# Kernel tuning notes

Hardware: AMD Instinct MI355X
Metric: run time of the kernel (lower is better)

Reference implementation:

```python
import jax, jax.numpy as jnp
import numpy as np

T = 1_000_000          # number of t_eval points (~1 year at 30 s)
N_ROOMS = 10
N = 12                 # 2 latent wall nodes + n_rooms
DT = 30.0              # seconds between t_eval points
LOAD_SCALE = 50.0      # physical_cooling_scaling: W/m^2 scale for sigmoid(loads)


def setup_inputs() -> dict:
    key = jax.random.key(0)
    k1, k2, k3, k4, k5 = jax.random.split(key, 5)
    t_eval = jnp.arange(T, dtype=jnp.float32) * DT
    x0 = 26.0 * jnp.ones((N,), jnp.float32)  # reset_iv: 26 C at every node
    # Stable slow RC dynamics: negative-definite-ish A with small coupling
    A = (-1e-5 * jnp.eye(N, dtype=jnp.float32)
         + 1e-6 * jax.random.normal(k1, (N, N), jnp.float32))
    B = 1e-6 * jax.random.normal(k2, (N, 1 + N_ROOMS), jnp.float32)
    Tout_data = 10.0 + 20.0 * jax.random.uniform(k3, (T,), jnp.float32)  # outdoor temp samples on t_eval grid
    loads_raw = jax.random.normal(k4, (2, N_ROOMS), jnp.float32)         # pre-sigmoid [cool; gain] loads
    room_areas = 10.0 + 40.0 * jax.random.uniform(k5, (N_ROOMS,), jnp.float32)
    return {"t_eval": t_eval, "x0": x0, "A": A, "B": B,
            "Tout_data": Tout_data, "loads_raw": loads_raw, "room_areas": room_areas}


def reference(t_eval, x0, A, B, Tout_data, loads_raw, room_areas):
    # transform + physical scaling of loads (self.transform = sigmoid)
    loads = jax.nn.sigmoid(loads_raw) * LOAD_SCALE
    cool_load, gain_load = loads[0], loads[1]
    action = 0.0  # no cooling policy -> self.action stays 0
    Q_area = -cool_load * action + gain_load            # [n_rooms]
    Q_watts = Q_area * room_areas                        # proportional_heating
    # u = [Tout; Q_watts] so B@u = B[:,0]*Tout + B[:,1:]@Q_watts (Q constant over t)
    b0 = B[:, 0]                                         # [N]
    Bq = B[:, 1:] @ Q_watts                              # [N], constant forcing
    h = t_eval[1] - t_eval[0]                            # uniform step
    # Linear interp of Tout: value at t_i, midpoint t_i+h/2, and t_{i+1}
    To_t = Tout_data[:-1]
    To_n = Tout_data[1:]
    To_m = 0.5 * (To_t + To_n)

    def f(x, To):  # dy/dt = A x + B u
        return A @ x + b0 * To + Bq

    def step(x, tou):
        to_t, to_m, to_n = tou
        k1 = f(x, to_t)
        k2 = f(x + 0.5 * h * k1, to_m)
        k3 = f(x + 0.5 * h * k2, to_m)
        k4 = f(x + h * k3, to_n)
        xn = x + (h / 6.0) * (k1 + 2.0 * k2 + 2.0 * k3 + k4)
        return xn, xn

    _, xs = jax.lax.scan(step, x0, (To_t, To_m, To_n))
    return jnp.concatenate([x0[None, :], xs], axis=0)  # [T, N]
```

## Files before the change

### kernel.cpp

```cpp
#include <hip/hip_runtime.h>
#include <math.h>


#define S_STEPS 999999
#define CH      8
#define BLK     512
#define NB      256
#define NLVL    9
#define NLOOK   16
#define NCHUNK  125000
#define LASTFULL 124998

#define OFF_MX  0
#define OFF_K   192
#define OFF_P2  312
#define OFF_PD  1608
#define OFF_AGG 3912
#define OFF_S   6984

__device__ inline void mm12(double* C, const double* A_, const double* B_, int t) {
  if (t < 144) {
    int i = t / 12, j = t % 12;
    double s = 0.0;
#pragma unroll
    for (int k = 0; k < 12; ++k) s += A_[i*12+k] * B_[k*12+j];
    C[t] = s;
  }
  __syncthreads();
}

__device__ inline void matvec12_s(const float* __restrict__ P,
                                  const float* in, float* out) {
#pragma unroll
  for (int i = 0; i < 12; ++i) {
    float acc = out[i];
#pragma unroll
    for (int j = 0; j < 12; ++j) acc = fmaf(P[i*12+j], in[j], acc);
    out[i] = acc;
  }
}

__global__ void setup_kernel(const float* __restrict__ t_eval,
                             const float* __restrict__ A,
                             const float* __restrict__ Bm,
                             const float* __restrict__ loads_raw,
                             const float* __restrict__ areas,
                             float* __restrict__ ws) {
  __shared__ double Md[144], T2[144], CUR[144], R4[144];
  __shared__ double H1[144], H2[144], H3[144], H4[144];
  __shared__ double cd[12], ald[12], bed[12], bqd[12], b0d[12];
  __shared__ double Kd[120];
  int t = threadIdx.x;
  double h = (double)t_eval[1] - (double)t_eval[0];
  if (t < 144) H1[t] = h * (double)A[t];
  if (t < 12) {
    b0d[t] = (double)Bm[t*11];
    double s = 0.0;
    for (int r = 0; r < 10; ++r) {
      double g = 50.0 / (1.0 + exp(-(double)loads_raw[10 + r]));
      s += (double)Bm[t*11 + 1 + r] * (g * (double)areas[r]);
    }
    bqd[t] = s;
  }
  if (t < 120) Kd[t] = 0.0;
  __syncthreads();
  mm12(H2, H1, H1, t);
  mm12(H3, H2, H1, t);
  mm12(H4, H2, H2, t);
  if (t < 12) {
    double hb=0,h2b=0,h3b=0,hb0=0,h2b0=0,h3b0=0;
    for (int k = 0; k < 12; ++k) {
      hb  += H1[t*12+k]*bqd[k]; h2b  += H2[t*12+k]*bqd[k]; h3b  += H3[t*12+k]*bqd[k];
      hb0 += H1[t*12+k]*b0d[k]; h2b0 += H2[t*12+k]*b0d[k]; h3b0 += H3[t*12+k]*b0d[k];
    }
    double h6 = h / 6.0;
    cd[t]  = h6*(6.0*bqd[t] + 3.0*hb + h2b + 0.25*h3b);
    ald[t] = h6*(3.0*b0d[t] + 2.0*hb0 + 0.75*h2b0 + 0.25*h3b0);
    bed[t] = h6*(3.0*b0d[t] + hb0 + 0.25*h2b0);
  }
  if (t < 144) {
    int i = t/12, j = t%12;
    Md[t] = (i==j ? 1.0 : 0.0) + H1[t] + 0.5*H2[t] + H3[t]/6.0 + H4[t]/24.0;
  }
  if (t < 144) CUR[t] = (t % 13 == 0) ? 1.0 : 0.0;
  __syncthreads();
  if (t < 192) {
    int i = t/16, j = t%16;
    float val = (j < 12) ? (float)Md[i*12+j]
              : (j == 12) ? (float)cd[i]
              : (j == 13) ? (float)ald[i]
              : (j == 14) ? (float)bed[i] : 0.f;
    ws[OFF_MX + t] = val;
  }
  for (int k = 0; k <= 8; ++k) {
    if (k > 0) {
      mm12(T2, CUR, Md, t);
      if (t < 144) CUR[t] = T2[t];
      __syncthreads();
    }
    if (t < 12 && k <= 7) {
      double sa=0, sb=0, sc=0;
      for (int j = 0; j < 12; ++j) {
        double m = CUR[t*12+j];
        sa += m*ald[j]; sb += m*bed[j]; sc += m*cd[j];
      }
      Kd[(8-k)*12 + t] += sa;
      Kd[(9-k)*12 + t] += sb;
      Kd[t]            += sc;
    }
    __syncthreads();
  }
  if (t < 120) ws[OFF_K + t] = (float)Kd[t];
  if (t < 144) ws[OFF_P2 + t] = (float)CUR[t];
  for (int l = 1; l <= 8; ++l) {
    mm12(T2, CUR, CUR, t);
    if (t < 144) CUR[t] = T2[t];
    __syncthreads();
    if (t < 144) ws[OFF_P2 + l*144 + t] = (float)CUR[t];
  }
  mm12(R4, CUR, CUR, t);
  if (t < 144) {
    ws[OFF_PD + t] = (t % 13 == 0) ? 1.f : 0.f;
    ws[OFF_PD + 144 + t] = (float)R4[t];
    CUR[t] = R4[t];
  }
  __syncthreads();
  for (int j = 2; j < NLOOK; ++j) {
    mm12(T2, CUR, R4, t);
    if (t < 144) CUR[t] = T2[t];
    __syncthreads();
    if (t < 144) ws[OFF_PD + j*144 + t] = (float)CUR[t];
  }
}

__global__ void __launch_bounds__(BLK) fold_scan(
    const float* __restrict__ cons, const float* __restrict__ To,
    const float* __restrict__ x0, float* __restrict__ sout,
    float* __restrict__ agg) {
  __shared__ float lw[BLK*13];
  int k = threadIdx.x, b = blockIdx.x;
  int g = b*BLK + k;
  int base = g*CH;
  bool fullc = (g <= LASTFULL);
  float to[9];
  if (fullc) {
    const float4* tp = reinterpret_cast<const float4*>(To + base);
    float4 a = tp[0], c = tp[1];
    to[0]=a.x; to[1]=a.y; to[2]=a.z; to[3]=a.w;
    to[4]=c.x; to[5]=c.y; to[6]=c.z; to[7]=c.w;
    to[8]=To[base+8];
  }
  float v[12];
  if (fullc) {
#pragma unroll
    for (int i = 0; i < 12; ++i) v[i] = cons[OFF_K + i];
#pragma unroll
    for (int s = 0; s < 9; ++s) {
      float ts = to[s];
#pragma unroll
      for (int i = 0; i < 12; ++i)
        v[i] = fmaf(cons[OFF_K + (s+1)*12 + i], ts, v[i]);
    }
  } else {
#pragma unroll
    for (int i = 0; i < 12; ++i) v[i] = 0.f;
  }
  if (g == 0) {
    float xi[12];
#pragma unroll
    for (int i = 0; i < 12; ++i) xi[i] = x0[i];
    matvec12_s(cons + OFF_P2, xi, v);
  }
#pragma unroll
  for (int i = 0; i < 12; ++i) lw[k*13+i] = v[i];
  __syncthreads();
#pragma unroll
  for (int l = 0; l < NLVL; ++l) {
    int off = 1 << l;
    float nb[12];
    bool act = (k >= off);
    if (act) {
#pragma unroll
      for (int i = 0; i < 12; ++i) nb[i] = lw[(k-off)*13 + i];
    }
    __syncthreads();
    if (act) {
      matvec12_s(cons + OFF_P2 + l*144, nb, v);
#pragma unroll
      for (int i = 0; i < 12; ++i) lw[k*13+i] = v[i];
    }
    __syncthreads();
  }
  float4* Sp = reinterpret_cast<float4*>(sout + (size_t)g*12);
  Sp[0] = make_float4(v[0],v[1],v[2],v[3]);
  Sp[1] = make_float4(v[4],v[5],v[6],v[7]);
  Sp[2] = make_float4(v[8],v[9],v[10],v[11]);
  if (k == BLK-1) {
#pragma unroll
    for (int i = 0; i < 12; ++i) agg[b*12 + i] = v[i];
  }
}

__global__ void __launch_bounds__(BLK) fixup_expand(
    const float* __restrict__ ws, const float* __restrict__ To,
    const float* __restrict__ x0, float* __restrict__ out) {
  __shared__ float partl[NLOOK*12];
  __shared__ float Xs[12];
  int k = threadIdx.x, b = blockIdx.x;
  int g = b*BLK + k;
  if (k < NLOOK*12) {
    int j = k/12, i = k%12, src = b - 1 - j;
    float acc = 0.f;
    if (src >= 0) {
#pragma unroll
      for (int m = 0; m < 12; ++m)
        acc = fmaf(ws[OFF_PD + j*144 + i*12 + m], ws[OFF_AGG + src*12 + m], acc);
    }
    partl[k] = acc;
  }
  __syncthreads();
  if (k < 12) {
    float s = 0.f;
#pragma unroll
    for (int j = 0; j < NLOOK; ++j) s += partl[j*12 + k];
    Xs[k] = s;
  }
  __syncthreads();
  float v[12];
#pragma unroll
  for (int i = 0; i < 12; ++i) v[i] = Xs[i];
#pragma unroll
  for (int l = 0; l < NLVL; ++l) {
    if ((k >> l) & 1) {
      float vn[12];
#pragma unroll
      for (int i = 0; i < 12; ++i) vn[i] = 0.f;
      matvec12_s(ws + OFF_P2 + l*144, v, vn);
#pragma unroll
      for (int i = 0; i < 12; ++i) v[i] = vn[i];
    }
  }
  float x[12];
  if (k > 0) {
    const float4* Sp = reinterpret_cast<const float4*>(ws + OFF_S + (size_t)(g-1)*12);
    float4 s0=Sp[0], s1=Sp[1], s2=Sp[2];
    x[0]=v[0]+s0.x; x[1]=v[1]+s0.y; x[2]=v[2]+s0.z; x[3]=v[3]+s0.w;
    x[4]=v[4]+s1.x; x[5]=v[5]+s1.y; x[6]=v[6]+s1.z; x[7]=v[7]+s1.w;
    x[8]=v[8]+s2.x; x[9]=v[9]+s2.y; x[10]=v[10]+s2.z; x[11]=v[11]+s2.w;
  } else {
#pragma unroll
    for (int i = 0; i < 12; ++i) x[i] = v[i] + (b == 0 ? x0[i] : 0.f);
  }
  if (b == 0 && k == 0) {
#pragma unroll
    for (int i = 0; i < 12; ++i) out[i] = x0[i];
  }
  if (g >= NCHUNK) return;
  int base = g*CH;
  float to[9];
  {
    const float4* tp = reinterpret_cast<const float4*>(To + base);
    float4 a = tp[0], c = tp[1];
    to[0]=a.x; to[1]=a.y; to[2]=a.z; to[3]=a.w;
    to[4]=c.x; to[5]=c.y; to[6]=c.z; to[7]=c.w;
    to[8] = (g <= LASTFULL) ? To[base+8] : 0.f;
  }
#pragma unroll
  for (int s = 0; s < CH; ++s) {
    int tt = base + s;
    if (tt >= S_STEPS) break;
    float tot = to[s], ton = to[s+1];
    float xn[12];
#pragma unroll
    for (int i = 0; i < 12; ++i) {
      const float* Mr = ws + OFF_MX + i*16;
      float acc = Mr[12];
      acc = fmaf(Mr[13], tot, acc);
      acc = fmaf(Mr[14], ton, acc);
#pragma unroll
      for (int m = 0; m < 12; ++m) acc = fmaf(Mr[m], x[m], acc);
      xn[i] = acc;
    }
    float4* op = reinterpret_cast<float4*>(out + (size_t)(tt+1)*12);
    op[0] = make_float4(xn[0],xn[1],xn[2],xn[3]);
    op[1] = make_float4(xn[4],xn[5],xn[6],xn[7]);
    op[2] = make_float4(xn[8],xn[9],xn[10],xn[11]);
#pragma unroll
    for (int i = 0; i < 12; ++i) x[i] = xn[i];
  }
}

extern "C" void kernel_launch(void* const* d_in, const int* in_sizes, int n_in,
                              void* d_out, int out_size, void* d_ws, size_t ws_size,
                              hipStream_t stream) {
  const float* t_eval    = (const float*)d_in[0];
  const float* x0        = (const float*)d_in[1];
  const float* A         = (const float*)d_in[2];
  const float* B         = (const float*)d_in[3];
  const float* To        = (const float*)d_in[4];
  const float* loads_raw = (const float*)d_in[5];
  const float* areas     = (const float*)d_in[6];
  float* out = (float*)d_out;
  float* ws  = (float*)d_ws;

  setup_kernel<<<1, 256, 0, stream>>>(t_eval, A, B, loads_raw, areas, ws);
  fold_scan<<<NB, BLK, 0, stream>>>(ws, To, x0, ws + OFF_S, ws + OFF_AGG);
  fixup_expand<<<NB, BLK, 0, stream>>>(ws, To, x0, out);
}
```

Measured before the change: 137.0 us.

## Drop intermediate scan buffer: recompute block scans and use wavefront shuffles

The first pass now computes only each block's aggregate. It uses wavefront shuffles and a small shared-memory tree instead of a full 9-level shared-memory scan, and it no longer writes per-chunk prefix states to global memory. The second pass recomputes the chunk folds and the in-block scan itself, and builds the carry-in for each 16-thread group from precomputed matrix powers. This cuts the prefix propagation chain per thread, and the per-step matrix is held in registers. The setup kernel is also parallelised across more threads. The trade is redundant fold work and higher register pressure in exchange for removing the global round-trip of the scan states.

Result: no change. 135.6 us (-1.1%).

```diff
diff --git a/kernel.cpp b/kernel.cpp
--- a/kernel.cpp
+++ b/kernel.cpp
@@ -6,50 +6,59 @@
 #define CH      8
 #define BLK     512
 #define NB      256
-#define NLVL    9
 #define NLOOK   16
 #define NCHUNK  125000
 #define LASTFULL 124998
 
-#define OFF_MX  0
+#define OFF_M   0
+#define OFF_C   144
+#define OFF_AL  156
+#define OFF_BE  168
 #define OFF_K   192
 #define OFF_P2  312
-#define OFF_PD  1608
-#define OFF_AGG 3912
-#define OFF_S   6984
-
-__device__ inline void mm12(double* C, const double* A_, const double* B_, int t) {
-  if (t < 144) {
-    int i = t / 12, j = t % 12;
-    double s = 0.0;
-#pragma unroll
-    for (int k = 0; k < 12; ++k) s += A_[i*12+k] * B_[k*12+j];
-    C[t] = s;
-  }
-  __syncthreads();
-}
-
-__device__ inline void matvec12_s(const float* __restrict__ P,
-                                  const float* in, float* out) {
+#define OFF_PQ  1608
+#define OFF_PW  2040
+#define OFF_PD  3048
+#define OFF_AGG 5352
+
+#define FMA4(Q,a,b,c,d,acc) fmaf((Q).w,(d),fmaf((Q).z,(c),fmaf((Q).y,(b),fmaf((Q).x,(a),(acc)))))
+
+__device__ __forceinline__ void mv_acc(const float* Pf, const float* x, float* y) {
+  const float4* P = reinterpret_cast<const float4*>(Pf);
 #pragma unroll
   for (int i = 0; i < 12; ++i) {
-    float acc = out[i];
-#pragma unroll
-    for (int j = 0; j < 12; ++j) acc = fmaf(P[i*12+j], in[j], acc);
-    out[i] = acc;
-  }
-}
-
-__global__ void setup_kernel(const float* __restrict__ t_eval,
-                             const float* __restrict__ A,
-                             const float* __restrict__ Bm,
-                             const float* __restrict__ loads_raw,
-                             const float* __restrict__ areas,
-                             float* __restrict__ ws) {
-  __shared__ double Md[144], T2[144], CUR[144], R4[144];
-  __shared__ double H1[144], H2[144], H3[144], H4[144];
-  __shared__ double cd[12], ald[12], bed[12], bqd[12], b0d[12];
-  __shared__ double Kd[120];
+    float4 a = P[3*i], b = P[3*i+1], c = P[3*i+2];
+    y[i] = FMA4(c, x[8],x[9],x[10],x[11],
+            FMA4(b, x[4],x[5],x[6],x[7],
+             FMA4(a, x[0],x[1],x[2],x[3], y[i])));
+  }
+}
+
+__device__ __forceinline__ void fold_chunk(const float* cons, const float* tos, float* v) {
+  const float4* Kq = reinterpret_cast<const float4*>(cons + OFF_K);
+  float4 c0=Kq[0], c1=Kq[1], c2=Kq[2];
+  v[0]=c0.x; v[1]=c0.y; v[2]=c0.z; v[3]=c0.w;
+  v[4]=c1.x; v[5]=c1.y; v[6]=c1.z; v[7]=c1.w;
+  v[8]=c2.x; v[9]=c2.y; v[10]=c2.z; v[11]=c2.w;
+#pragma unroll
+  for (int s = 0; s < 9; ++s) {
+    float ts = tos[s];
+    float4 ka=Kq[3*(s+1)], kb=Kq[3*(s+1)+1], kc=Kq[3*(s+1)+2];
+    v[0]=fmaf(ka.x,ts,v[0]); v[1]=fmaf(ka.y,ts,v[1]); v[2]=fmaf(ka.z,ts,v[2]); v[3]=fmaf(ka.w,ts,v[3]);
+    v[4]=fmaf(kb.x,ts,v[4]); v[5]=fmaf(kb.y,ts,v[5]); v[6]=fmaf(kb.z,ts,v[6]); v[7]=fmaf(kb.w,ts,v[7]);
+    v[8]=fmaf(kc.x,ts,v[8]); v[9]=fmaf(kc.y,ts,v[9]); v[10]=fmaf(kc.z,ts,v[10]); v[11]=fmaf(kc.w,ts,v[11]);
+  }
+}
+
+__global__ void __launch_bounds__(512) setup_kernel(
+    const float* __restrict__ t_eval, const float* __restrict__ A,
+    const float* __restrict__ Bm, const float* __restrict__ loads_raw,
+    const float* __restrict__ areas, float* ws) {
+  __shared__ double H1[144], H2[144], H3[144], H4[144], Md[144];
+  __shared__ double Qa[144], Qb[144], D1536[144];
+  __shared__ double C128[144], C256[144], C512[144], C1024[144], C2048[144], C4096[144];
+  __shared__ double cd[12], ald[12], bed[12], b0d[12], bqd[12];
+  __shared__ double Vv[3][12], Kd[120];
   int t = threadIdx.x;
   double h = (double)t_eval[1] - (double)t_eval[0];
   if (t < 144) H1[t] = h * (double)A[t];
@@ -57,110 +66,143 @@
     b0d[t] = (double)Bm[t*11];
     double s = 0.0;
     for (int r = 0; r < 10; ++r) {
-      double g = 50.0 / (1.0 + exp(-(double)loads_raw[10 + r]));
-      s += (double)Bm[t*11 + 1 + r] * (g * (double)areas[r]);
+      double gq = 50.0 / (1.0 + exp(-(double)loads_raw[10 + r]));
+      s += (double)Bm[t*11 + 1 + r] * (gq * (double)areas[r]);
     }
     bqd[t] = s;
   }
   if (t < 120) Kd[t] = 0.0;
   __syncthreads();
-  mm12(H2, H1, H1, t);
-  mm12(H3, H2, H1, t);
-  mm12(H4, H2, H2, t);
+  if (t < 144) {
+    int i=t/12, j=t%12; double s=0.0;
+#pragma unroll
+    for (int m = 0; m < 12; ++m) s += H1[i*12+m]*H1[m*12+j];
+    H2[t]=s;
+  }
+  __syncthreads();
+  if (t < 288) {
+    int w=t/144, e=t%144, i=e/12, j=e%12;
+    const double* Bp = w ? H2 : H1;
+    double s = 0.0;
+#pragma unroll
+    for (int m = 0; m < 12; ++m) s += H2[i*12+m]*Bp[m*12+j];
+    (w ? H4 : H3)[e] = s;
+  }
+  __syncthreads();
   if (t < 12) {
     double hb=0,h2b=0,h3b=0,hb0=0,h2b0=0,h3b0=0;
-    for (int k = 0; k < 12; ++k) {
-      hb  += H1[t*12+k]*bqd[k]; h2b  += H2[t*12+k]*bqd[k]; h3b  += H3[t*12+k]*bqd[k];
-      hb0 += H1[t*12+k]*b0d[k]; h2b0 += H2[t*12+k]*b0d[k]; h3b0 += H3[t*12+k]*b0d[k];
+#pragma unroll
+    for (int m = 0; m < 12; ++m) {
+      hb  += H1[t*12+m]*bqd[m]; h2b  += H2[t*12+m]*bqd[m]; h3b  += H3[t*12+m]*bqd[m];
+      hb0 += H1[t*12+m]*b0d[m]; h2b0 += H2[t*12+m]*b0d[m]; h3b0 += H3[t*12+m]*b0d[m];
     }
     double h6 = h / 6.0;
     cd[t]  = h6*(6.0*bqd[t] + 3.0*hb + h2b + 0.25*h3b);
     ald[t] = h6*(3.0*b0d[t] + 2.0*hb0 + 0.75*h2b0 + 0.25*h3b0);
     bed[t] = h6*(3.0*b0d[t] + hb0 + 0.25*h2b0);
-  }
+    Vv[0][t]=ald[t]; Vv[1][t]=bed[t]; Vv[2][t]=cd[t];
+    Kd[96+t] += ald[t]; Kd[108+t] += bed[t]; Kd[t] += cd[t];
+  }
+  if (t >= 144 && t < 288) {
+    int e=t-144, i=e/12, j=e%12;
+    Md[e] = (i==j ? 1.0 : 0.0) + H1[e] + 0.5*H2[e] + H3[e]/6.0 + H4[e]/24.0;
+  }
+  __syncthreads();
+  if (t < 144) { ws[OFF_M+t] = (float)Md[t]; Qa[t] = Md[t]; }
+  if (t < 12) {
+    ws[OFF_C+t]=(float)cd[t]; ws[OFF_AL+t]=(float)ald[t]; ws[OFF_BE+t]=(float)bed[t];
+  }
+  __syncthreads();
+  double* src = Qa; double* dst = Qb;
+  for (int r = 1; r <= 12; ++r) {
+    double acc = 0.0, ks = 0.0;
+    if (t < 144) {
+      int i=t/12, j=t%12;
+#pragma unroll
+      for (int m = 0; m < 12; ++m) acc += src[i*12+m]*src[m*12+j];
+    }
+    int w=0, i2=0;
+    if (r <= 7 && t >= 256 && t < 292) {
+      w=(t-256)/12; i2=(t-256)%12;
+#pragma unroll
+      for (int m = 0; m < 12; ++m) ks += Md[i2*12+m]*Vv[w][m];
+    }
+    __syncthreads();
+    if (t < 144) {
+      dst[t] = acc;
+      if (r >= 3 && r <= 11) ws[OFF_P2+(r-3)*144+t] = (float)acc;
+      if (r == 7)  C128[t]=acc;
+      if (r == 8)  C256[t]=acc;
+      if (r == 9)  C512[t]=acc;
+      if (r == 10) C1024[t]=acc;
+      if (r == 11) C2048[t]=acc;
+      if (r == 12) C4096[t]=acc;
+    }
+    if (r <= 7 && t >= 256 && t < 292) {
+      Vv[w][i2] = ks;
+      if (w == 0) Kd[(8-r)*12+i2] += ks;
+      else if (w == 1) Kd[(9-r)*12+i2] += ks;
+      else Kd[i2] += ks;
+    }
+    __syncthreads();
+    double* tmp = src; src = dst; dst = tmp;
+  }
+  if (t < 120) ws[OFF_K+t] = (float)Kd[t];
   if (t < 144) {
-    int i = t/12, j = t%12;
-    Md[t] = (i==j ? 1.0 : 0.0) + H1[t] + 0.5*H2[t] + H3[t]/6.0 + H4[t]/24.0;
-  }
-  if (t < 144) CUR[t] = (t % 13 == 0) ? 1.0 : 0.0;
-  __syncthreads();
-  if (t < 192) {
-    int i = t/16, j = t%16;
-    float val = (j < 12) ? (float)Md[i*12+j]
-              : (j == 12) ? (float)cd[i]
-              : (j == 13) ? (float)ald[i]
-              : (j == 14) ? (float)bed[i] : 0.f;
-    ws[OFF_MX + t] = val;
-  }
-  for (int k = 0; k <= 8; ++k) {
-    if (k > 0) {
-      mm12(T2, CUR, Md, t);
-      if (t < 144) CUR[t] = T2[t];
-      __syncthreads();
-    }
-    if (t < 12 && k <= 7) {
-      double sa=0, sb=0, sc=0;
-      for (int j = 0; j < 12; ++j) {
-        double m = CUR[t*12+j];
-        sa += m*ald[j]; sb += m*bed[j]; sc += m*cd[j];
-      }
-      Kd[(8-k)*12 + t] += sa;
-      Kd[(9-k)*12 + t] += sb;
-      Kd[t]            += sc;
-    }
-    __syncthreads();
-  }
-  if (t < 120) ws[OFF_K + t] = (float)Kd[t];
-  if (t < 144) ws[OFF_P2 + t] = (float)CUR[t];
-  for (int l = 1; l <= 8; ++l) {
-    mm12(T2, CUR, CUR, t);
-    if (t < 144) CUR[t] = T2[t];
-    __syncthreads();
-    if (t < 144) ws[OFF_P2 + l*144 + t] = (float)CUR[t];
-  }
-  mm12(R4, CUR, CUR, t);
-  if (t < 144) {
-    ws[OFF_PD + t] = (t % 13 == 0) ? 1.f : 0.f;
-    ws[OFF_PD + 144 + t] = (float)R4[t];
-    CUR[t] = R4[t];
-  }
-  __syncthreads();
+    ws[OFF_PQ+t]       = (float)C128[t];
+    ws[OFF_PQ+144+t]   = (float)C256[t];
+    ws[OFF_PW+t]       = (float)C512[t];
+    ws[OFF_PW+144+t]   = (float)C1024[t];
+    ws[OFF_PW+3*144+t] = (float)C2048[t];
+    ws[OFF_PD+t]       = (t % 13 == 0) ? 1.f : 0.f;
+    ws[OFF_PD+144+t]   = (float)C4096[t];
+  }
+  if (t < 432) {
+    int w=t/144, e=t%144, i=e/12, j=e%12;
+    const double* Ap = (w==0) ? C128 : C512;
+    const double* Bp = (w==0) ? C256 : ((w==1) ? C1024 : C2048);
+    double s = 0.0;
+#pragma unroll
+    for (int m = 0; m < 12; ++m) s += Ap[i*12+m]*Bp[m*12+j];
+    if (w==0) ws[OFF_PQ+2*144+e] = (float)s;
+    else if (w==1) { D1536[e]=s; ws[OFF_PW+2*144+e] = (float)s; }
+    else ws[OFF_PW+4*144+e] = (float)s;
+  }
+  __syncthreads();
+  if (t < 288) {
+    int w=t/144, e=t%144, i=e/12, j=e%12;
+    const double* Ap = (w==0) ? C1024 : D1536;
+    double s = 0.0;
+#pragma unroll
+    for (int m = 0; m < 12; ++m) s += Ap[i*12+m]*C2048[m*12+j];
+    ws[OFF_PW+((w==0)?5:6)*144+e] = (float)s;
+  }
   for (int j = 2; j < NLOOK; ++j) {
-    mm12(T2, CUR, R4, t);
-    if (t < 144) CUR[t] = T2[t];
-    __syncthreads();
-    if (t < 144) ws[OFF_PD + j*144 + t] = (float)CUR[t];
-  }
-}
-
-__global__ void __launch_bounds__(BLK) fold_scan(
-    const float* __restrict__ cons, const float* __restrict__ To,
-    const float* __restrict__ x0, float* __restrict__ sout,
-    float* __restrict__ agg) {
-  __shared__ float lw[BLK*13];
+    double acc = 0.0;
+    if (t < 144) {
+      int i=t/12, jj=t%12;
+#pragma unroll
+      for (int m = 0; m < 12; ++m) acc += src[i*12+m]*C4096[m*12+jj];
+    }
+    __syncthreads();
+    if (t < 144) { dst[t] = acc; ws[OFF_PD+j*144+t] = (float)acc; }
+    __syncthreads();
+    double* tmp = src; src = dst; dst = tmp;
+  }
+}
+
+__global__ void __launch_bounds__(BLK) block_agg(
+    const float* cons, const float* __restrict__ To,
+    const float* __restrict__ x0, float* agg) {
+  __shared__ float Tw[96], Ta[48], Tb[24];
   int k = threadIdx.x, b = blockIdx.x;
-  int g = b*BLK + k;
-  int base = g*CH;
-  bool fullc = (g <= LASTFULL);
-  float to[9];
-  if (fullc) {
+  int g = b*BLK + k, base = g*CH;
+  float v[12];
+  if (g <= LASTFULL) {
     const float4* tp = reinterpret_cast<const float4*>(To + base);
-    float4 a = tp[0], c = tp[1];
-    to[0]=a.x; to[1]=a.y; to[2]=a.z; to[3]=a.w;
-    to[4]=c.x; to[5]=c.y; to[6]=c.z; to[7]=c.w;
-    to[8]=To[base+8];
-  }
-  float v[12];
-  if (fullc) {
-#pragma unroll
-    for (int i = 0; i < 12; ++i) v[i] = cons[OFF_K + i];
-#pragma unroll
-    for (int s = 0; s < 9; ++s) {
-      float ts = to[s];
-#pragma unroll
-      for (int i = 0; i < 12; ++i)
-        v[i] = fmaf(cons[OFF_K + (s+1)*12 + i], ts, v[i]);
-    }
+    float4 ta = tp[0], tb = tp[1];
+    float tos[9] = {ta.x,ta.y,ta.z,ta.w, tb.x,tb.y,tb.z,tb.w, To[base+8]};
+    fold_chunk(cons, tos, v);
   } else {
 #pragma unroll
     for (int i = 0; i < 12; ++i) v[i] = 0.f;
@@ -169,52 +211,103 @@
     float xi[12];
 #pragma unroll
     for (int i = 0; i < 12; ++i) xi[i] = x0[i];
-    matvec12_s(cons + OFF_P2, xi, v);
-  }
-#pragma unroll
-  for (int i = 0; i < 12; ++i) lw[k*13+i] = v[i];
-  __syncthreads();
-#pragma unroll
-  for (int l = 0; l < NLVL; ++l) {
+    mv_acc(cons + OFF_P2, xi, v);
+  }
+#pragma unroll
+  for (int l = 0; l < 6; ++l) {
     int off = 1 << l;
     float nb[12];
-    bool act = (k >= off);
-    if (act) {
-#pragma unroll
-      for (int i = 0; i < 12; ++i) nb[i] = lw[(k-off)*13 + i];
-    }
-    __syncthreads();
-    if (act) {
-      matvec12_s(cons + OFF_P2 + l*144, nb, v);
-#pragma unroll
-      for (int i = 0; i < 12; ++i) lw[k*13+i] = v[i];
-    }
-    __syncthreads();
-  }
-  float4* Sp = reinterpret_cast<float4*>(sout + (size_t)g*12);
-  Sp[0] = make_float4(v[0],v[1],v[2],v[3]);
-  Sp[1] = make_float4(v[4],v[5],v[6],v[7]);
-  Sp[2] = make_float4(v[8],v[9],v[10],v[11]);
-  if (k == BLK-1) {
-#pragma unroll
-    for (int i = 0; i < 12; ++i) agg[b*12 + i] = v[i];
-  }
-}
-
-__global__ void __launch_bounds__(BLK) fixup_expand(
-    const float* __restrict__ ws, const float* __restrict__ To,
+#pragma unroll
+    for (int i = 0; i < 12; ++i) nb[i] = __shfl_up(v[i], (unsigned)off, 64);
+    if ((k & 63) >= off) mv_acc(cons + OFF_P2 + l*144, nb, v);
+  }
+  if ((k & 63) == 63) {
+#pragma unroll
+    for (int i = 0; i < 12; ++i) Tw[(k>>6)*12 + i] = v[i];
+  }
+  __syncthreads();
+  if (k < 48) {
+    int p = k/12, i = k%12;
+    const float* L = Tw + 2*p*12;
+    float acc = Tw[(2*p+1)*12 + i];
+    const float4* Pr = reinterpret_cast<const float4*>(cons + OFF_P2 + 6*144 + i*12);
+    float4 p0=Pr[0], p1=Pr[1], p2=Pr[2];
+    acc = FMA4(p0, L[0],L[1],L[2],L[3], acc);
+    acc = FMA4(p1, L[4],L[5],L[6],L[7], acc);
+    acc = FMA4(p2, L[8],L[9],L[10],L[11], acc);
+    Ta[p*12+i] = acc;
+  }
+  __syncthreads();
+  if (k < 24) {
+    int q = k/12, i = k%12;
+    const float* L = Ta + 2*q*12;
+    float acc = Ta[(2*q+1)*12 + i];
+    const float4* Pr = reinterpret_cast<const float4*>(cons + OFF_P2 + 7*144 + i*12);
+    float4 p0=Pr[0], p1=Pr[1], p2=Pr[2];
+    acc = FMA4(p0, L[0],L[1],L[2],L[3], acc);
+    acc = FMA4(p1, L[4],L[5],L[6],L[7], acc);
+    acc = FMA4(p2, L[8],L[9],L[10],L[11], acc);
+    Tb[q*12+i] = acc;
+  }
+  __syncthreads();
+  if (k < 12) {
+    float acc = Tb[12 + k];
+    const float4* Pr = reinterpret_cast<const float4*>(cons + OFF_P2 + 8*144 + k*12);
+    float4 p0=Pr[0], p1=Pr[1], p2=Pr[2];
+    acc = FMA4(p0, Tb[0],Tb[1],Tb[2],Tb[3], acc);
+    acc = FMA4(p1, Tb[4],Tb[5],Tb[6],Tb[7], acc);
+    acc = FMA4(p2, Tb[8],Tb[9],Tb[10],Tb[11], acc);
+    agg[b*12 + k] = acc;
+  }
+}
+
+#define ROWX(i, MA,MB,MC) xn[i] = FMA4(MC, x[8],x[9],x[10],x[11], \
+    FMA4(MB, x[4],x[5],x[6],x[7], FMA4(MA, x[0],x[1],x[2],x[3], \
+    fmaf(bv[i],ton,fmaf(av[i],tot,cv[i])))));
+
+__global__ void __launch_bounds__(BLK, 2) scan_expand(
+    const float* cons, const float* __restrict__ To,
     const float* __restrict__ x0, float* __restrict__ out) {
+  __shared__ float lw[BLK*13];
   __shared__ float partl[NLOOK*12];
   __shared__ float Xs[12];
+  __shared__ float Xw[96];
+  __shared__ float Xq[384];
   int k = threadIdx.x, b = blockIdx.x;
-  int g = b*BLK + k;
+  int g = b*BLK + k, base = g*CH;
+  bool active = (g < NCHUNK), fullc = (g <= LASTFULL);
+  float to[9];
+  if (active) {
+    const float4* tp = reinterpret_cast<const float4*>(To + base);
+    float4 ta = tp[0], tb = tp[1];
+    to[0]=ta.x; to[1]=ta.y; to[2]=ta.z; to[3]=ta.w;
+    to[4]=tb.x; to[5]=tb.y; to[6]=tb.z; to[7]=tb.w;
+    to[8] = fullc ? To[base+8] : 0.f;
+  }
+  float v[12];
+  if (fullc) fold_chunk(cons, to, v);
+  else {
+#pragma unroll
+    for (int i = 0; i < 12; ++i) v[i] = 0.f;
+  }
+  if (g == 0) {
+    float xi[12];
+#pragma unroll
+    for (int i = 0; i < 12; ++i) xi[i] = x0[i];
+    mv_acc(cons + OFF_P2, xi, v);
+  }
+#pragma unroll
+  for (int i = 0; i < 12; ++i) lw[k*13+i] = v[i];
   if (k < NLOOK*12) {
     int j = k/12, i = k%12, src = b - 1 - j;
     float acc = 0.f;
     if (src >= 0) {
-#pragma unroll
-      for (int m = 0; m < 12; ++m)
-        acc = fmaf(ws[OFF_PD + j*144 + i*12 + m], ws[OFF_AGG + src*12 + m], acc);
+      const float4* Pr = reinterpret_cast<const float4*>(cons + OFF_PD + j*144 + i*12);
+      const float4* Ar = reinterpret_cast<const float4*>(cons + OFF_AGG + src*12);
+      float4 p0=Pr[0], p1=Pr[1], p2=Pr[2], a0=Ar[0], a1=Ar[1], a2=Ar[2];
+      acc = FMA4(p0, a0.x,a0.y,a0.z,a0.w, acc);
+      acc = FMA4(p1, a1.x,a1.y,a1.z,a1.w, acc);
+      acc = FMA4(p2, a2.x,a2.y,a2.z,a2.w, acc);
     }
     partl[k] = acc;
   }
@@ -225,62 +318,125 @@
     for (int j = 0; j < NLOOK; ++j) s += partl[j*12 + k];
     Xs[k] = s;
   }
-  __syncthreads();
-  float v[12];
-#pragma unroll
-  for (int i = 0; i < 12; ++i) v[i] = Xs[i];
-#pragma unroll
-  for (int l = 0; l < NLVL; ++l) {
+#pragma unroll
+  for (int l = 0; l < 9; ++l) {
+    int off = 1 << l;
+    bool act = (k >= off);
+    float nb[12];
+    if (act) {
+#pragma unroll
+      for (int i = 0; i < 12; ++i) nb[i] = lw[(k-off)*13 + i];
+    }
+    __syncthreads();
+    if (act) {
+      mv_acc(cons + OFF_P2 + l*144, nb, v);
+#pragma unroll
+      for (int i = 0; i < 12; ++i) lw[k*13+i] = v[i];
+    }
+    __syncthreads();
+  }
+  float sp[12];
+  if (k > 0) {
+#pragma unroll
+    for (int i = 0; i < 12; ++i) sp[i] = lw[(k-1)*13 + i];
+  } else {
+#pragma unroll
+    for (int i = 0; i < 12; ++i) sp[i] = 0.f;
+  }
+  if (k < 96) {
+    int w = k/12, i = k%12;
+    float acc;
+    if (w == 0) acc = Xs[i];
+    else {
+      const float4* Wr = reinterpret_cast<const float4*>(cons + OFF_PW + (w-1)*144 + i*12);
+      float4 p0=Wr[0], p1=Wr[1], p2=Wr[2];
+      acc = FMA4(p0, Xs[0],Xs[1],Xs[2],Xs[3], 0.f);
+      acc = FMA4(p1, Xs[4],Xs[5],Xs[6],Xs[7], acc);
+      acc = FMA4(p2, Xs[8],Xs[9],Xs[10],Xs[11], acc);
+    }
+    Xw[w*12 + i] = acc;
+  }
+  __syncthreads();
+  if (k < 384) {
+    int q = k/12, i = k%12, d = q & 3;
+    const float* xw = Xw + (q>>2)*12;
+    float acc;
+    if (d == 0) acc = xw[i];
+    else {
+      const float4* Qr = reinterpret_cast<const float4*>(cons + OFF_PQ + (d-1)*144 + i*12);
+      float4 p0=Qr[0], p1=Qr[1], p2=Qr[2];
+      acc = FMA4(p0, xw[0],xw[1],xw[2],xw[3], 0.f);
+      acc = FMA4(p1, xw[4],xw[5],xw[6],xw[7], acc);
+      acc = FMA4(p2, xw[8],xw[9],xw[10],xw[11], acc);
+    }
+    Xq[q*12 + i] = acc;
+  }
+  __syncthreads();
+  float vp[12];
+  {
+    const float* xq = Xq + (k>>4)*12;
+#pragma unroll
+    for (int i = 0; i < 12; ++i) vp[i] = xq[i];
+  }
+#pragma unroll
+  for (int l = 0; l < 4; ++l) {
     if ((k >> l) & 1) {
       float vn[12];
 #pragma unroll
       for (int i = 0; i < 12; ++i) vn[i] = 0.f;
-      matvec12_s(ws + OFF_P2 + l*144, v, vn);
-#pragma unroll
-      for (int i = 0; i < 12; ++i) v[i] = vn[i];
+      mv_acc(cons + OFF_P2 + l*144, vp, vn);
+#pragma unroll
+      for (int i = 0; i < 12; ++i) vp[i] = vn[i];
     }
   }
   float x[12];
   if (k > 0) {
-    const float4* Sp = reinterpret_cast<const float4*>(ws + OFF_S + (size_t)(g-1)*12);
-    float4 s0=Sp[0], s1=Sp[1], s2=Sp[2];
-    x[0]=v[0]+s0.x; x[1]=v[1]+s0.y; x[2]=v[2]+s0.z; x[3]=v[3]+s0.w;
-    x[4]=v[4]+s1.x; x[5]=v[5]+s1.y; x[6]=v[6]+s1.z; x[7]=v[7]+s1.w;
-    x[8]=v[8]+s2.x; x[9]=v[9]+s2.y; x[10]=v[10]+s2.z; x[11]=v[11]+s2.w;
+#pragma unroll
+    for (int i = 0; i < 12; ++i) x[i] = vp[i] + sp[i];
   } else {
 #pragma unroll
-    for (int i = 0; i < 12; ++i) x[i] = v[i] + (b == 0 ? x0[i] : 0.f);
+    for (int i = 0; i < 12; ++i) x[i] = vp[i] + (b == 0 ? x0[i] : 0.f);
   }
   if (b == 0 && k == 0) {
 #pragma unroll
     for (int i = 0; i < 12; ++i) out[i] = x0[i];
   }
-  if (g >= NCHUNK) return;
-  int base = g*CH;
-  float to[9];
+  if (!active) return;
+  float cv[12], av[12], bv[12];
   {
-    const float4* tp = reinterpret_cast<const float4*>(To + base);
-    float4 a = tp[0], c = tp[1];
-    to[0]=a.x; to[1]=a.y; to[2]=a.z; to[3]=a.w;
-    to[4]=c.x; to[5]=c.y; to[6]=c.z; to[7]=c.w;
-    to[8] = (g <= LASTFULL) ? To[base+8] : 0.f;
-  }
+    const float4* Cq = reinterpret_cast<const float4*>(cons + OFF_C);
+    const float4* Aq = reinterpret_cast<const float4*>(cons + OFF_AL);
+    const float4* Bq = reinterpret_cast<const float4*>(cons + OFF_BE);
+    float4 q;
+    q=Cq[0]; cv[0]=q.x;cv[1]=q.y;cv[2]=q.z;cv[3]=q.w;
+    q=Cq[1]; cv[4]=q.x;cv[5]=q.y;cv[6]=q.z;cv[7]=q.w;
+    q=Cq[2]; cv[8]=q.x;cv[9]=q.y;cv[10]=q.z;cv[11]=q.w;
+    q=Aq[0]; av[0]=q.x;av[1]=q.y;av[2]=q.z;av[3]=q.w;
+    q=Aq[1]; av[4]=q.x;av[5]=q.y;av[6]=q.z;av[7]=q.w;
+    q=Aq[2]; av[8]=q.x;av[9]=q.y;av[10]=q.z;av[11]=q.w;
+    q=Bq[0]; bv[0]=q.x;bv[1]=q.y;bv[2]=q.z;bv[3]=q.w;
+    q=Bq[1]; bv[4]=q.x;bv[5]=q.y;bv[6]=q.z;bv[7]=q.w;
+    q=Bq[2]; bv[8]=q.x;bv[9]=q.y;bv[10]=q.z;bv[11]=q.w;
+  }
+  const float4* Mq = reinterpret_cast<const float4*>(cons + OFF_M);
+  float4 m00=Mq[0],  m01=Mq[1],  m02=Mq[2],  m03=Mq[3],  m04=Mq[4],  m05=Mq[5];
+  float4 m06=Mq[6],  m07=Mq[7],  m08=Mq[8],  m09=Mq[9],  m10=Mq[10], m11=Mq[11];
+  float4 m12=Mq[12], m13=Mq[13], m14=Mq[14], m15=Mq[15], m16=Mq[16], m17=Mq[17];
+  float4 m18=Mq[18], m19=Mq[19], m20=Mq[20], m21=Mq[21], m22=Mq[22], m23=Mq[23];
+  float4 m24=Mq[24], m25=Mq[25], m26=Mq[26], m27=Mq[27], m28=Mq[28], m29=Mq[29];
+  float4 m30=Mq[30], m31=Mq[31], m32=Mq[32], m33=Mq[33], m34=Mq[34], m35=Mq[35];
 #pragma unroll
   for (int s = 0; s < CH; ++s) {
     int tt = base + s;
     if (tt >= S_STEPS) break;
     float tot = to[s], ton = to[s+1];
     float xn[12];
-#pragma unroll
-    for (int i = 0; i < 12; ++i) {
-      const float* Mr = ws + OFF_MX + i*16;
-      float acc = Mr[12];
-      acc = fmaf(Mr[13], tot, acc);
-      acc = fmaf(Mr[14], ton, acc);
-#pragma unroll
-      for (int m = 0; m < 12; ++m) acc = fmaf(Mr[m], x[m], acc);
-      xn[i] = acc;
-    }
+    ROWX(0,  m00,m01,m02)  ROWX(1,  m03,m04,m05)
+    ROWX(2,  m06,m07,m08)  ROWX(3,  m09,m10,m11)
+    ROWX(4,  m12,m13,m14)  ROWX(5,  m15,m16,m17)
+    ROWX(6,  m18,m19,m20)  ROWX(7,  m21,m22,m23)
+    ROWX(8,  m24,m25,m26)  ROWX(9,  m27,m28,m29)
+    ROWX(10, m30,m31,m32)  ROWX(11, m33,m34,m35)
     float4* op = reinterpret_cast<float4*>(out + (size_t)(tt+1)*12);
     op[0] = make_float4(xn[0],xn[1],xn[2],xn[3]);
     op[1] = make_float4(xn[4],xn[5],xn[6],xn[7]);
@@ -303,7 +459,7 @@
   float* out = (float*)d_out;
   float* ws  = (float*)d_ws;
 
-  setup_kernel<<<1, 256, 0, stream>>>(t_eval, A, B, loads_raw, areas, ws);
-  fold_scan<<<NB, BLK, 0, stream>>>(ws, To, x0, ws + OFF_S, ws + OFF_AGG);
-  fixup_expand<<<NB, BLK, 0, stream>>>(ws, To, x0, out);
-}
+  setup_kernel<<<1, 512, 0, stream>>>(t_eval, A, B, loads_raw, areas, ws);
+  block_agg<<<NB, BLK, 0, stream>>>(ws, To, x0, ws + OFF_AGG);
+  scan_expand<<<NB, BLK, 0, stream>>>(ws, To, x0, out);
+}
```
